# Performance work log

Measured on AMD Instinct MI355X. Metric: run time of the kernel, lower is better.

Reference implementation:

```python
import jax, jax.numpy as jnp
import numpy as np

ALPHA = 0.2  # tf.nn.leaky_relu default alpha
B, LATENT, T, N = 8, 256, 128, 768
F, L, E = 4, 3, 12288


def _causal_conv1d(x, w, b):
    # x: [B,T,Cin], w: [K,Cin,Cout] -> causal pad left by K-1
    k = w.shape[0]
    y = jax.lax.conv_general_dilated(x, w, (1,), ((k - 1, 0),),
                                     dimension_numbers=('NWC', 'WIO', 'NWC'))
    return y + b


def _same_conv1d(x, w, b):
    y = jax.lax.conv_general_dilated(x, w, (1,), 'SAME',
                                     dimension_numbers=('NWC', 'WIO', 'NWC'))
    return y + b


def _same_conv2d(x, w, b):
    y = jax.lax.conv_general_dilated(x, w, (1, 1), 'SAME',
                                     dimension_numbers=('NHWC', 'HWIO', 'NHWC'))
    return y + b


def _gat(nodes, row, col, qw, qb, kw, kb, vw, vb):
    # tf_geometric-style single-head GAT; row/col already contain self-loops.
    M = nodes.shape[0]
    Q = jax.nn.leaky_relu(nodes @ qw + qb, ALPHA)
    K = jax.nn.leaky_relu(nodes @ kw + kb, ALPHA)
    V = nodes @ vw
    scale = jnp.sqrt(jnp.asarray(Q.shape[-1], nodes.dtype))
    score = jnp.sum(Q[row] * K[col], axis=-1) / scale  # [E']
    smax = jax.ops.segment_max(score, row, num_segments=M)
    ex = jnp.exp(score - smax[row])
    den = jax.ops.segment_sum(ex, row, num_segments=M)
    att = ex / den[row]
    out = jax.ops.segment_sum(V[col] * att[:, None], row, num_segments=M)
    return out + vb


def _gw_layer(y, row, col, wa, ba, wb, bb, qw, qb, kw, kb, vw, vb, rw, rb):
    b_, t_, n_, f_ = y.shape
    x = jnp.moveaxis(y, -1, 0)  # [F,B,T,N]

    def branch(xf, wa_, ba_, wb_, bb_, qw_, qb_, kw_, kb_, vw_, vb_):
        a = jax.nn.sigmoid(_causal_conv1d(xf, wa_, ba_))
        g = a * jnp.tanh(_causal_conv1d(xf, wb_, bb_))   # gated TCN [B,T,N]
        nodes = g.transpose(0, 2, 1).reshape(b_ * n_, t_)  # node id = b*N + n
        h = _gat(nodes, row, col, qw_, qb_, kw_, kb_, vw_, vb_)
        return h.reshape(b_, n_, t_).transpose(0, 2, 1)  # [B,T,N]

    outs = jax.vmap(branch)(x, wa, ba, wb, bb, qw, qb, kw, kb, vw, vb)
    outs = jnp.moveaxis(outs, 0, -1)                      # [B,T,N,F]
    res = jnp.einsum('btnf,fg->btng', y, rw) + rb         # 1x1 res conv
    return outs + res


def _decoder(x, edges, shunt_dense_w, shunt_dense_b, shunt_c1_w, shunt_c1_b,
             shunt_c2_w, shunt_c2_b, tcn_a_w, tcn_a_b, tcn_b_w, tcn_b_b,
             gat_q_w, gat_q_b, gat_k_w, gat_k_b, gat_v_w, gat_v_b,
             res_w, res_b, skip_w, skip_b, out1_w, out1_b, out2_w, out2_b):
    # ConvShunt: [B,latent] -> [B,T] -> [B,T,N] -> [B,T,N,F]
    y = x @ shunt_dense_w + shunt_dense_b
    y = _same_conv1d(y[..., None], shunt_c1_w, shunt_c1_b)
    y = _same_conv2d(y[..., None], shunt_c2_w, shunt_c2_b)
    M = B * N
    self_idx = jnp.arange(M, dtype=edges.dtype)
    row = jnp.concatenate([edges[0], self_idx])
    col = jnp.concatenate([edges[1], self_idx])
    skips = []
    for i in range(L):
        y = _gw_layer(y, row, col, tcn_a_w[i], tcn_a_b[i], tcn_b_w[i], tcn_b_b[i],
                      gat_q_w[i], gat_q_b[i], gat_k_w[i], gat_k_b[i],
                      gat_v_w[i], gat_v_b[i], res_w[i], res_b[i])
        skips.append(jax.nn.leaky_relu(
            jnp.einsum('btnf,f->btn', y, skip_w[i]) + skip_b[i], ALPHA))
    s = jnp.stack(skips, axis=-1)                         # [B,T,N,L]
    g = jax.nn.leaky_relu(_same_conv2d(s, out1_w, out1_b), ALPHA)
    return _same_conv2d(g, out2_w, out2_b)                # [B,T,N,1]


def setup_inputs() -> dict:
    ks = iter(jax.random.split(jax.random.key(0), 32))

    def w(shape, fan_in):
        return jax.random.normal(next(ks), shape, jnp.float32) / np.sqrt(fan_in).astype(np.float32)

    return {
        'x': jax.random.normal(next(ks), (B, LATENT), jnp.float32),
        'edges': jax.random.randint(next(ks), (2, E), 0, N, jnp.int32),
        'shunt_dense_w': w((LATENT, T), LATENT),
        'shunt_dense_b': jnp.zeros((T,), jnp.float32),
        'shunt_c1_w': w((3, 1, N), 3),
        'shunt_c1_b': jnp.zeros((N,), jnp.float32),
        'shunt_c2_w': w((3, 3, 1, F), 9),
        'shunt_c2_b': jnp.zeros((F,), jnp.float32),
        'tcn_a_w': w((L, F, 5, N, N), 5 * N),
        'tcn_a_b': jnp.zeros((L, F, N), jnp.float32),
        'tcn_b_w': w((L, F, 5, N, N), 5 * N),
        'tcn_b_b': jnp.zeros((L, F, N), jnp.float32),
        'gat_q_w': w((L, F, T, T), T),
        'gat_q_b': jnp.zeros((L, F, T), jnp.float32),
        'gat_k_w': w((L, F, T, T), T),
        'gat_k_b': jnp.zeros((L, F, T), jnp.float32),
        'gat_v_w': w((L, F, T, T), T),
        'gat_v_b': jnp.zeros((L, F, T), jnp.float32),
        'res_w': w((L, F, F), F),
        'res_b': jnp.zeros((L, F), jnp.float32),
        'skip_w': w((L, F), F),
        'skip_b': jnp.zeros((L,), jnp.float32),
        'out1_w': w((3, 3, L, 1), 9 * L),
        'out1_b': jnp.zeros((1,), jnp.float32),
        'out2_w': w((1, 1, 1, 1), 1),
        'out2_b': jnp.zeros((1,), jnp.float32),
    }


def reference(x, edges, shunt_dense_w, shunt_dense_b, shunt_c1_w, shunt_c1_b,
              shunt_c2_w, shunt_c2_b, tcn_a_w, tcn_a_b, tcn_b_w, tcn_b_b,
              gat_q_w, gat_q_b, gat_k_w, gat_k_b, gat_v_w, gat_v_b,
              res_w, res_b, skip_w, skip_b, out1_w, out1_b, out2_w, out2_b):
    return _decoder(x, edges, shunt_dense_w, shunt_dense_b, shunt_c1_w, shunt_c1_b,
                    shunt_c2_w, shunt_c2_b, tcn_a_w, tcn_a_b, tcn_b_w, tcn_b_b,
                    gat_q_w, gat_q_b, gat_k_w, gat_k_b, gat_v_w, gat_v_b,
                    res_w, res_b, skip_w, skip_b, out1_w, out1_b, out2_w, out2_b)
```

## Files before the change

### kernel.cpp

```cpp
#include <hip/hip_runtime.h>
#include <math.h>

#define ALPHA_ 0.2f
#define AS1 __attribute__((address_space(1)))
#define AS3 __attribute__((address_space(3)))

constexpr int B_ = 8, LATENT_ = 256, T_ = 128, N_ = 768, F_ = 4, L_ = 3, E_ = 12288;
constexpr int M_ = B_ * N_;
constexpr int MT_ = B_ * T_;
constexpr int EP_ = E_ + M_;
constexpr int BTN_ = B_ * T_ * N_;
constexpr size_t SZ_ = (size_t)BTN_ * F_;
constexpr int KTCN_ = 5 * N_;
constexpr int KSPLIT_ = KTCN_ / 2;
constexpr int TP_ = T_ + 4;

typedef __bf16 bf16x8 __attribute__((ext_vector_type(8)));
typedef float f32x4 __attribute__((ext_vector_type(4)));

__device__ __forceinline__ float lrelu(float x) { return x > 0.0f ? x : ALPHA_ * x; }
__device__ __forceinline__ unsigned short f2bf(float x) {
    union { __bf16 h; unsigned short u; } c; c.h = (__bf16)x; return c.u;
}
__device__ __forceinline__ float bf2f(unsigned short u) {
    return __uint_as_float(((unsigned)u) << 16);
}

__global__ void k_dense(const float* __restrict__ x, const float* __restrict__ w,
                        const float* __restrict__ b, float* __restrict__ y0) {
    int i = blockIdx.x * blockDim.x + threadIdx.x;
    if (i >= B_ * T_) return;
    int bb = i / T_, t = i % T_;
    float acc = b[t];
    for (int l = 0; l < LATENT_; ++l) acc += x[bb * LATENT_ + l] * w[l * T_ + t];
    y0[i] = acc;
}

__global__ void k_conv1(const float* __restrict__ y0, const float* __restrict__ w,
                        const float* __restrict__ b, float* __restrict__ y1) {
    int i = blockIdx.x * blockDim.x + threadIdx.x;
    if (i >= BTN_) return;
    int n = i % N_, t = (i / N_) % T_, bb = i / (N_ * T_);
    float acc = b[n];
    #pragma unroll
    for (int k = 0; k < 3; ++k) {
        int tt = t - 1 + k;
        if (tt >= 0 && tt < T_) acc += y0[bb * T_ + tt] * w[k * N_ + n];
    }
    y1[i] = acc;
}

__global__ void k_conv2w(const float* __restrict__ y1, const float* __restrict__ w,
                         const float* __restrict__ b, float* __restrict__ y,
                         unsigned short* __restrict__ xTpad) {
    int i = blockIdx.x * blockDim.x + threadIdx.x;
    if (i >= BTN_) return;
    int n = i % N_, t = (i / N_) % T_, bb = i / (N_ * T_);
    float acc[F_];
    #pragma unroll
    for (int f = 0; f < F_; ++f) acc[f] = b[f];
    #pragma unroll
    for (int dt = 0; dt < 3; ++dt) {
        int tt = t - 1 + dt;
        if (tt < 0 || tt >= T_) continue;
        #pragma unroll
        for (int dn = 0; dn < 3; ++dn) {
            int nn = n - 1 + dn;
            if (nn < 0 || nn >= N_) continue;
            float v = y1[(bb * T_ + tt) * N_ + nn];
            #pragma unroll
            for (int f = 0; f < F_; ++f) acc[f] += v * w[(dt * 3 + dn) * F_ + f];
        }
    }
    #pragma unroll
    for (int f = 0; f < F_; ++f) {
        y[(size_t)i * F_ + f] = acc[f];
        xTpad[((size_t)(f * B_ + bb) * TP_ + 4 + t) * N_ + n] = f2bf(acc[f]);
    }
}

__global__ __launch_bounds__(256) void k_convT2(const float* __restrict__ aw,
        const float* __restrict__ bw, unsigned short* __restrict__ wat3,
        unsigned short* __restrict__ wbt3) {
    __shared__ float tl[64][33];
    const int z = blockIdx.z;
    const int f = z & 3, wsel = (z >> 2) & 1, layer = z >> 3;
    const size_t toff = ((size_t)layer * F_ + f) * KTCN_ * N_;
    const float* in = (wsel ? bw : aw) + toff;
    unsigned short* outT = (wsel ? wbt3 : wat3) + toff;
    const int n0 = blockIdx.x * 32, k0 = blockIdx.y * 64;
    const int tx = threadIdx.x & 31, ty = threadIdx.x >> 5;
    #pragma unroll
    for (int r = 0; r < 8; ++r)
        tl[ty + r * 8][tx] = in[(size_t)(k0 + ty + r * 8) * N_ + n0 + tx];
    __syncthreads();
    const int kx2 = threadIdx.x & 63, ny = threadIdx.x >> 6;
    #pragma unroll
    for (int r = 0; r < 8; ++r)
        outT[(size_t)(n0 + ny + r * 4) * KTCN_ + k0 + kx2] = f2bf(tl[kx2][ny + r * 4]);
}

__global__ __launch_bounds__(256) void k_convTproj(const float* __restrict__ qw,
        const float* __restrict__ kw, const float* __restrict__ vw,
        unsigned short* __restrict__ pwt3) {
    __shared__ float tl[32][33];
    const int z = blockIdx.z;
    const int f = z & 3;
    const int sel = (z >> 2) % 3;
    const int layer = z / 12;
    const float* in = (sel == 0 ? qw : (sel == 1 ? kw : vw))
                      + ((size_t)layer * F_ + f) * T_ * T_;
    unsigned short* outT = pwt3 + (((size_t)layer * 3 + sel) * F_ + f) * T_ * T_;
    const int x0 = blockIdx.x * 32;
    const int y0 = blockIdx.y * 32;
    const int tx = threadIdx.x & 31, ty = threadIdx.x >> 5;
    #pragma unroll
    for (int r = 0; r < 4; ++r)
        tl[ty + r * 8][tx] = in[(size_t)(y0 + ty + r * 8) * T_ + x0 + tx];
    __syncthreads();
    #pragma unroll
    for (int r = 0; r < 4; ++r)
        outT[(size_t)(x0 + ty + r * 8) * T_ + y0 + tx] = f2bf(tl[tx][ty + r * 8]);
}

__global__ __launch_bounds__(256) void k_tcn_mfma(
        const unsigned short* __restrict__ xTpad,
        const unsigned short* __restrict__ wat, const unsigned short* __restrict__ wbt,
        const float* __restrict__ ba, const float* __restrict__ bbias,
        unsigned short* __restrict__ oa0, unsigned short* __restrict__ oa1,
        unsigned short* __restrict__ ob0, unsigned short* __restrict__ ob1) {
    __shared__ unsigned short As[128 * 32];
    __shared__ unsigned short Bs[128 * 32];
    const int bid = blockIdx.x;
    const int bt = bid / 96;
    const int c = bid - bt * 96;
    const int xb = c % 6;
    const int zz = c / 6;
    const int f = zz & 3;
    const int wsel = (zz >> 2) & 1;
    const int s = zz >> 3;
    const int n0 = xb * 128;
    const unsigned short* xf = xTpad + (size_t)(f * B_ + bt) * TP_ * N_;
    const unsigned short* wf = (wsel ? wbt : wat) + (size_t)f * N_ * KTCN_ + (size_t)n0 * KTCN_;
    const float* bias = (wsel ? bbias : ba) + f * N_;
    unsigned short* out = (wsel ? (s ? ob1 : ob0) : (s ? oa1 : oa0));
    const int tid = threadIdx.x;
    const int lane = tid & 63;
    const int w = tid >> 6;
    const int wm = (w >> 1) * 64, wn = (w & 1) * 64;
    const int r16 = lane & 15, kb = lane >> 4;
    const int srow = lane >> 2;
    const int scol = (((lane & 3) ^ ((lane >> 3) & 3)) * 8);
    const int kx = (kb ^ ((r16 >> 1) & 3)) * 8;
    f32x4 acc[4][4] = {};
    const int k_lo = s * KSPLIT_, k_hi = k_lo + KSPLIT_;
    for (int kk0 = k_lo; kk0 < k_hi; kk0 += 32) {
        const int ks = kk0 / N_;
        const int nin0 = kk0 - ks * N_;
        #pragma unroll
        for (int h = 0; h < 2; ++h) {
            const int seg = w + 4 * h;
            const int row = seg * 16 + srow;
            const unsigned short* gA = xf + (size_t)(row + ks) * N_ + nin0 + scol;
            const unsigned short* gB = wf + (size_t)row * KTCN_ + kk0 + scol;
            __builtin_amdgcn_global_load_lds((const AS1 unsigned int*)(const void*)gA,
                    (AS3 unsigned int*)(void*)(As + seg * 512), 16, 0, 0);
            __builtin_amdgcn_global_load_lds((const AS1 unsigned int*)(const void*)gB,
                    (AS3 unsigned int*)(void*)(Bs + seg * 512), 16, 0, 0);
        }
        __syncthreads();
        bf16x8 av[4], bv[4];
        #pragma unroll
        for (int i = 0; i < 4; ++i) av[i] = *(const bf16x8*)(As + (wm + i * 16 + r16) * 32 + kx);
        #pragma unroll
        for (int j = 0; j < 4; ++j) bv[j] = *(const bf16x8*)(Bs + (wn + j * 16 + r16) * 32 + kx);
        #pragma unroll
        for (int i = 0; i < 4; ++i)
            #pragma unroll
            for (int j = 0; j < 4; ++j)
                acc[i][j] = __builtin_amdgcn_mfma_f32_16x16x32_bf16(av[i], bv[j], acc[i][j], 0, 0, 0);
        __syncthreads();
    }
    unsigned short* of = out + (size_t)(f * B_ + bt) * T_ * N_;
    #pragma unroll
    for (int i = 0; i < 4; ++i) {
        #pragma unroll
        for (int j = 0; j < 4; ++j) {
            const int n = n0 + wn + j * 16 + r16;
            const float bv2 = (s == 0) ? bias[n] : 0.0f;
            #pragma unroll
            for (int r = 0; r < 4; ++r) {
                const int m = wm + i * 16 + kb * 4 + r;
                of[(size_t)m * N_ + n] = f2bf(acc[i][j][r] + bv2);
            }
        }
    }
}

__global__ __launch_bounds__(256) void k_gate_nodes(const unsigned short* __restrict__ a0,
        const unsigned short* __restrict__ a1, const unsigned short* __restrict__ b0,
        const unsigned short* __restrict__ b1, unsigned short* __restrict__ nodes) {
    __shared__ float tl[32][33];
    const int bz = blockIdx.z;
    const int t0 = blockIdx.x * 32, n0 = blockIdx.y * 32;
    const int tx = threadIdx.x & 31, ty = threadIdx.x >> 5;
    const size_t base = (size_t)bz * T_ * N_;
    #pragma unroll
    for (int r = 0; r < 4; ++r) {
        const size_t idx = base + (size_t)(t0 + ty + r * 8) * N_ + n0 + tx;
        const float av = bf2f(a0[idx]) + bf2f(a1[idx]);
        const float bvv = bf2f(b0[idx]) + bf2f(b1[idx]);
        tl[ty + r * 8][tx] = (1.0f / (1.0f + __expf(-av))) * tanhf(bvv);
    }
    __syncthreads();
    #pragma unroll
    for (int r = 0; r < 4; ++r)
        nodes[base + (size_t)(n0 + ty + r * 8) * T_ + t0 + tx] = f2bf(tl[tx][ty + r * 8]);
}

__global__ __launch_bounds__(256) void k_proj_mfma(
        const unsigned short* __restrict__ nodes, const unsigned short* __restrict__ pwt,
        const float* __restrict__ qb, const float* __restrict__ kbias,
        unsigned short* __restrict__ Q, unsigned short* __restrict__ K,
        unsigned short* __restrict__ V) {
    __shared__ unsigned short As[128 * 32];
    __shared__ unsigned short Bs[128 * 32];
    const int zz = blockIdx.z;
    const int f = zz & 3;
    const int sel = zz >> 2;
    const int m0 = blockIdx.y * 128;
    const unsigned short* af = nodes + (size_t)f * M_ * T_;
    const unsigned short* wfp = pwt + (size_t)sel * F_ * T_ * T_ + (size_t)f * T_ * T_;
    const float* bias = (sel == 0) ? qb : (sel == 1 ? kbias : nullptr);
    unsigned short* out = (sel == 0) ? Q : (sel == 1 ? K : V);
    const int tid = threadIdx.x;
    const int lane = tid & 63;
    const int w = tid >> 6;
    const int wm = (w >> 1) * 64, wn = (w & 1) * 64;
    const int r16 = lane & 15, kb = lane >> 4;
    const int srow = lane >> 2;
    const int scol = (((lane & 3) ^ ((lane >> 3) & 3)) * 8);
    const int kx = (kb ^ ((r16 >> 1) & 3)) * 8;
    f32x4 acc[4][4] = {};
    for (int kk0 = 0; kk0 < T_; kk0 += 32) {
        #pragma unroll
        for (int h = 0; h < 2; ++h) {
            const int seg = w + 4 * h;
            const int row = seg * 16 + srow;
            const unsigned short* gA = af + (size_t)(m0 + row) * T_ + kk0 + scol;
            const unsigned short* gB = wfp + (size_t)row * T_ + kk0 + scol;
            __builtin_amdgcn_global_load_lds((const AS1 unsigned int*)(const void*)gA,
                    (AS3 unsigned int*)(void*)(As + seg * 512), 16, 0, 0);
            __builtin_amdgcn_global_load_lds((const AS1 unsigned int*)(const void*)gB,
                    (AS3 unsigned int*)(void*)(Bs + seg * 512), 16, 0, 0);
        }
        __syncthreads();
        bf16x8 av[4], bv[4];
        #pragma unroll
        for (int i = 0; i < 4; ++i) av[i] = *(const bf16x8*)(As + (wm + i * 16 + r16) * 32 + kx);
        #pragma unroll
        for (int j = 0; j < 4; ++j) bv[j] = *(const bf16x8*)(Bs + (wn + j * 16 + r16) * 32 + kx);
        #pragma unroll
        for (int i = 0; i < 4; ++i)
            #pragma unroll
            for (int j = 0; j < 4; ++j)
                acc[i][j] = __builtin_amdgcn_mfma_f32_16x16x32_bf16(av[i], bv[j], acc[i][j], 0, 0, 0);
        __syncthreads();
    }
    const int do_l = (sel < 2);
    unsigned short* of = out + (size_t)f * M_ * T_;
    #pragma unroll
    for (int i = 0; i < 4; ++i) {
        #pragma unroll
        for (int j = 0; j < 4; ++j) {
            const int n = wn + j * 16 + r16;
            #pragma unroll
            for (int r = 0; r < 4; ++r) {
                const int m = m0 + wm + i * 16 + kb * 4 + r;
                float v = acc[i][j][r];
                if (bias) v += bias[f * T_ + n];
                if (do_l) v = lrelu(v);
                of[(size_t)m * T_ + n] = f2bf(v);
            }
        }
    }
}

__device__ __forceinline__ int edge_row(const int* e, int i) { return i < E_ ? e[i] : i - E_; }
__device__ __forceinline__ int edge_col(const int* e, int i) { return i < E_ ? e[E_ + i] : i - E_; }

__global__ void k_hist(const int* __restrict__ edges, int* __restrict__ deg) {
    int i = blockIdx.x * blockDim.x + threadIdx.x;
    if (i >= EP_) return;
    atomicAdd(&deg[edge_row(edges, i)], 1);
}

__global__ __launch_bounds__(256) void k_scan(const int* __restrict__ deg,
        int* __restrict__ rowptr, int* __restrict__ cursor) {
    __shared__ int part[256];
    const int tid = threadIdx.x;
    constexpr int PER = M_ / 256;
    int loc[PER];
    int s = 0;
    #pragma unroll
    for (int j = 0; j < PER; ++j) { loc[j] = s; s += deg[tid * PER + j]; }
    part[tid] = s;
    __syncthreads();
    if (tid == 0) {
        int run = 0;
        for (int i2 = 0; i2 < 256; ++i2) { int v = part[i2]; part[i2] = run; run += v; }
        rowptr[M_] = run;
    }
    __syncthreads();
    const int off = part[tid];
    #pragma unroll
    for (int j = 0; j < PER; ++j) {
        rowptr[tid * PER + j] = off + loc[j];
        cursor[tid * PER + j] = off + loc[j];
    }
}

__global__ void k_scatter(const int* __restrict__ edges, int* __restrict__ cursor,
                          int* __restrict__ csr_col) {
    int i = blockIdx.x * blockDim.x + threadIdx.x;
    if (i >= EP_) return;
    int r = edge_row(edges, i), c = edge_col(edges, i);
    int pos = atomicAdd(&cursor[r], 1);
    csr_col[pos] = c;
}

__global__ __launch_bounds__(256) void k_gat(const unsigned short* __restrict__ Q,
        const unsigned short* __restrict__ Kb, const unsigned short* __restrict__ V,
        const int* __restrict__ rowptr, const int* __restrict__ csr_col,
        unsigned short* __restrict__ H) {
    constexpr int CAP = 128;
    __shared__ float sc[4][CAP];
    const int w = threadIdx.x >> 6, lane = threadIdx.x & 63;
    const int wv = blockIdx.x * 4 + w;
    const int f = wv / M_, r = wv - f * M_;
    const int p0 = rowptr[r], p1 = rowptr[r + 1];
    const unsigned short* Qr = Q + ((size_t)f * M_ + r) * T_;
    const float q0 = bf2f(Qr[lane]), q1 = bf2f(Qr[lane + 64]);
    float mx = -3.4e38f;
    for (int j = p0; j < p1; ++j) {
        const unsigned short* Kc = Kb + ((size_t)f * M_ + csr_col[j]) * T_;
        float s = q0 * bf2f(Kc[lane]) + q1 * bf2f(Kc[lane + 64]);
        #pragma unroll
        for (int mk = 32; mk >= 1; mk >>= 1) s += __shfl_xor(s, mk);
        s *= 0.0883883476483184f;
        if (lane == 0 && j - p0 < CAP) sc[w][j - p0] = s;
        mx = fmaxf(mx, s);
    }
    float den = 0.0f;
    for (int j = p0; j < p1; ++j) {
        float s;
        if (j - p0 < CAP) s = sc[w][j - p0];
        else {
            const unsigned short* Kc = Kb + ((size_t)f * M_ + csr_col[j]) * T_;
            s = q0 * bf2f(Kc[lane]) + q1 * bf2f(Kc[lane + 64]);
            #pragma unroll
            for (int mk = 32; mk >= 1; mk >>= 1) s += __shfl_xor(s, mk);
            s *= 0.0883883476483184f;
        }
        den += __expf(s - mx);
    }
    const float rden = 1.0f / den;
    float a0 = 0.0f, a1 = 0.0f;
    for (int j = p0; j < p1; ++j) {
        const int c = csr_col[j];
        float s;
        if (j - p0 < CAP) s = sc[w][j - p0];
        else {
            const unsigned short* Kc = Kb + ((size_t)f * M_ + c) * T_;
            s = q0 * bf2f(Kc[lane]) + q1 * bf2f(Kc[lane + 64]);
            #pragma unroll
            for (int mk = 32; mk >= 1; mk >>= 1) s += __shfl_xor(s, mk);
            s *= 0.0883883476483184f;
        }
        const float att = __expf(s - mx) * rden;
        const unsigned short* Vc = V + ((size_t)f * M_ + c) * T_;
        a0 += att * bf2f(Vc[lane]);
        a1 += att * bf2f(Vc[lane + 64]);
    }
    unsigned short* Hr = H + ((size_t)f * M_ + r) * T_;
    Hr[lane] = f2bf(a0);
    Hr[lane + 64] = f2bf(a1);
}

__global__ __launch_bounds__(256) void k_combine_t(const float* __restrict__ y,
        const unsigned short* __restrict__ H, const float* __restrict__ vb,
        const float* __restrict__ rw, const float* __restrict__ rb,
        const float* __restrict__ skw, const float* __restrict__ skb, int layer,
        float* __restrict__ ynext, unsigned short* __restrict__ xTpad,
        float* __restrict__ sbufp) {
    __shared__ float hl[F_][32][33];
    const int b = blockIdx.z;
    const int t0 = blockIdx.x * 32, n0 = blockIdx.y * 32;
    const int tx = threadIdx.x & 31, ty = threadIdx.x >> 5;
    #pragma unroll
    for (int g = 0; g < F_; ++g)
        #pragma unroll
        for (int r = 0; r < 4; ++r) {
            const int nn = ty + r * 8;
            hl[g][nn][tx] = bf2f(H[((size_t)g * M_ + b * N_ + n0 + nn) * T_ + t0 + tx]);
        }
    __syncthreads();
    #pragma unroll
    for (int r = 0; r < 4; ++r) {
        const int tt = ty + r * 8;
        const int t = t0 + tt;
        const size_t i = ((size_t)b * T_ + t) * N_ + n0 + tx;
        const float4 y4 = *(const float4*)(y + i * 4);
        float o[F_];
        #pragma unroll
        for (int g = 0; g < F_; ++g) {
            float acc = hl[g][tx][tt] + vb[g * T_ + t] + rb[g];
            acc += y4.x * rw[0 * F_ + g] + y4.y * rw[1 * F_ + g]
                 + y4.z * rw[2 * F_ + g] + y4.w * rw[3 * F_ + g];
            o[g] = acc;
        }
        float4 o4 = {o[0], o[1], o[2], o[3]};
        *(float4*)(ynext + i * 4) = o4;
        #pragma unroll
        for (int g = 0; g < F_; ++g)
            xTpad[((size_t)(g * B_ + b) * TP_ + 4 + t) * N_ + n0 + tx] = f2bf(o[g]);
        float sk = skb[layer];
        #pragma unroll
        for (int g = 0; g < F_; ++g) sk += o[g] * skw[layer * F_ + g];
        sbufp[(size_t)layer * BTN_ + i] = lrelu(sk);
    }
}

__global__ void k_final(const float* __restrict__ sbufp, const float* __restrict__ o1w,
        const float* __restrict__ o1b, const float* __restrict__ o2w,
        const float* __restrict__ o2b, float* __restrict__ out) {
    int i = blockIdx.x * blockDim.x + threadIdx.x;
    if (i >= BTN_) return;
    int n = i % N_, t = (i / N_) % T_, bb = i / (N_ * T_);
    float acc = o1b[0];
    #pragma unroll
    for (int dt = 0; dt < 3; ++dt) {
        int tt = t - 1 + dt;
        if (tt < 0 || tt >= T_) continue;
        #pragma unroll
        for (int dn = 0; dn < 3; ++dn) {
            int nn = n - 1 + dn;
            if (nn < 0 || nn >= N_) continue;
            const size_t base = (size_t)(bb * T_ + tt) * N_ + nn;
            #pragma unroll
            for (int l = 0; l < L_; ++l)
                acc += sbufp[(size_t)l * BTN_ + base] * o1w[(dt * 3 + dn) * L_ + l];
        }
    }
    float g = lrelu(acc);
    out[i] = g * o2w[0] + o2b[0];
}

extern "C" void kernel_launch(void* const* d_in, const int* in_sizes, int n_in,
                              void* d_out, int out_size, void* d_ws, size_t ws_size,
                              hipStream_t stream) {
    const float* x       = (const float*)d_in[0];
    const int*   edges   = (const int*)d_in[1];
    const float* sd_w    = (const float*)d_in[2];
    const float* sd_b    = (const float*)d_in[3];
    const float* c1w     = (const float*)d_in[4];
    const float* c1b     = (const float*)d_in[5];
    const float* c2w     = (const float*)d_in[6];
    const float* c2b     = (const float*)d_in[7];
    const float* tcn_a_w = (const float*)d_in[8];
    const float* tcn_a_b = (const float*)d_in[9];
    const float* tcn_b_w = (const float*)d_in[10];
    const float* tcn_b_b = (const float*)d_in[11];
    const float* gat_q_w = (const float*)d_in[12];
    const float* gat_q_b = (const float*)d_in[13];
    const float* gat_k_w = (const float*)d_in[14];
    const float* gat_k_b = (const float*)d_in[15];
    const float* gat_v_w = (const float*)d_in[16];
    const float* gat_v_b = (const float*)d_in[17];
    const float* res_w   = (const float*)d_in[18];
    const float* res_b   = (const float*)d_in[19];
    const float* skip_w  = (const float*)d_in[20];
    const float* skip_b  = (const float*)d_in[21];
    const float* out1_w  = (const float*)d_in[22];
    const float* out1_b  = (const float*)d_in[23];
    const float* out2_w  = (const float*)d_in[24];
    const float* out2_b  = (const float*)d_in[25];
    float* out = (float*)d_out;

    float* ws = (float*)d_ws;
    size_t off = 0;
    auto alloc = [&](size_t nf) { float* p = ws + off; off += nf; return p; };
    float* ybuf  = alloc(SZ_);
    float* y2buf = alloc(SZ_);
    float* sbufp = alloc((size_t)BTN_ * L_);
    float* y0    = alloc(MT_);
    float* y1    = alloc(BTN_);
    unsigned short* xTpad  = (unsigned short*)alloc((size_t)F_ * B_ * TP_ * N_ / 2 + 16);
    unsigned short* nodesb = (unsigned short*)alloc(SZ_ / 2);
    unsigned short* qb16   = (unsigned short*)alloc(SZ_ / 2);
    unsigned short* kb16   = (unsigned short*)alloc(SZ_ / 2);
    unsigned short* vb16   = (unsigned short*)alloc(SZ_ / 2);
    unsigned short* Hb     = (unsigned short*)alloc(SZ_ / 2);
    unsigned short* pa0    = (unsigned short*)alloc(SZ_ / 2);
    unsigned short* pa1    = (unsigned short*)alloc(SZ_ / 2);
    unsigned short* pb0    = (unsigned short*)alloc(SZ_ / 2);
    unsigned short* pb1    = (unsigned short*)alloc(SZ_ / 2);
    unsigned short* wat3 = (unsigned short*)alloc((size_t)L_ * F_ * KTCN_ * N_ / 2);
    unsigned short* wbt3 = (unsigned short*)alloc((size_t)L_ * F_ * KTCN_ * N_ / 2);
    unsigned short* pwt3 = (unsigned short*)alloc((size_t)L_ * 3 * F_ * T_ * T_ / 2);
    int* rowptr  = (int*)alloc(M_ + 1);
    int* cursor  = (int*)alloc(M_);
    int* deg     = (int*)alloc(M_);
    int* csr_col = (int*)alloc(EP_);
    (void)ws_size; (void)in_sizes; (void)n_in; (void)out_size;

    hipMemsetAsync(xTpad, 0, (size_t)F_ * B_ * TP_ * N_ * 2, stream);
    hipMemsetAsync(deg, 0, M_ * 4, stream);
    k_hist<<<(EP_ + 255) / 256, 256, 0, stream>>>(edges, deg);
    k_scan<<<1, 256, 0, stream>>>(deg, rowptr, cursor);
    k_scatter<<<(EP_ + 255) / 256, 256, 0, stream>>>(edges, cursor, csr_col);

    dim3 gw2(N_ / 32, KTCN_ / 64, 8 * L_);
    k_convT2<<<gw2, 256, 0, stream>>>(tcn_a_w, tcn_b_w, wat3, wbt3);
    dim3 gpw(T_ / 32, T_ / 32, 12 * L_);
    k_convTproj<<<gpw, 256, 0, stream>>>(gat_q_w, gat_k_w, gat_v_w, pwt3);

    k_dense<<<(B_ * T_ + 255) / 256, 256, 0, stream>>>(x, sd_w, sd_b, y0);
    k_conv1<<<(BTN_ + 255) / 256, 256, 0, stream>>>(y0, c1w, c1b, y1);
    k_conv2w<<<(BTN_ + 255) / 256, 256, 0, stream>>>(y1, c2w, c2b, ybuf, xTpad);

    float* cur = ybuf;
    float* nxt = y2buf;
    for (int layer = 0; layer < L_; ++layer) {
        const float* ba = tcn_a_b + (size_t)layer * F_ * N_;
        const float* bb = tcn_b_b + (size_t)layer * F_ * N_;
        const float* qb = gat_q_b + (size_t)layer * F_ * T_;
        const float* kbias = gat_k_b + (size_t)layer * F_ * T_;
        const float* vb = gat_v_b + (size_t)layer * F_ * T_;
        const float* rw = res_w + (size_t)layer * F_ * F_;
        const float* rb = res_b + (size_t)layer * F_;
        const unsigned short* wat = wat3 + (size_t)layer * F_ * KTCN_ * N_;
        const unsigned short* wbt = wbt3 + (size_t)layer * F_ * KTCN_ * N_;
        const unsigned short* pwt = pwt3 + (size_t)layer * 3 * F_ * T_ * T_;

        k_tcn_mfma<<<768, 256, 0, stream>>>(xTpad, wat, wbt, ba, bb, pa0, pa1, pb0, pb1);
        dim3 gg(T_ / 32, N_ / 32, F_ * B_);
        k_gate_nodes<<<gg, 256, 0, stream>>>(pa0, pa1, pb0, pb1, nodesb);
        dim3 gp(1, M_ / 128, 12);
        k_proj_mfma<<<gp, 256, 0, stream>>>(nodesb, pwt, qb, kbias, qb16, kb16, vb16);
        k_gat<<<(F_ * M_) / 4, 256, 0, stream>>>(qb16, kb16, vb16, rowptr, csr_col, Hb);
        dim3 gc(T_ / 32, N_ / 32, B_);
        k_combine_t<<<gc, 256, 0, stream>>>(cur, Hb, vb, rw, rb, skip_w, skip_b,
                layer, nxt, xTpad, sbufp);
        float* tmp = cur; cur = nxt; nxt = tmp;
    }
    k_final<<<(BTN_ + 255) / 256, 256, 0, stream>>>(sbufp, out1_w, out1_b, out2_w, out2_b, out);
}
```

Baseline: 577.5 us.

## Split TCN GEMM K dimension four ways and vectorize weight transpose

The TCN MFMA kernel now splits its K reduction into four parts instead of two, doubling the grid to 1536 blocks so more CUs have work. The gate kernel sums four bf16 partials per element, which adds partial-buffer write and read traffic. The weight transpose kernel is also reworked to use 64x64 tiles with float4 loads and 16-byte packed bf16 stores, cutting the number of memory transactions in that one-time conversion.

Result: slower. 610.6 us (+5.7%).

```diff
diff --git a/kernel.cpp b/kernel.cpp
--- a/kernel.cpp
+++ b/kernel.cpp
@@ -12,7 +12,7 @@
 constexpr int BTN_ = B_ * T_ * N_;
 constexpr size_t SZ_ = (size_t)BTN_ * F_;
 constexpr int KTCN_ = 5 * N_;
-constexpr int KSPLIT_ = KTCN_ / 2;
+constexpr int KS4_ = KTCN_ / 4;
 constexpr int TP_ = T_ + 4;
 
 typedef __bf16 bf16x8 __attribute__((ext_vector_type(8)));
@@ -82,22 +82,36 @@
 __global__ __launch_bounds__(256) void k_convT2(const float* __restrict__ aw,
         const float* __restrict__ bw, unsigned short* __restrict__ wat3,
         unsigned short* __restrict__ wbt3) {
-    __shared__ float tl[64][33];
+    __shared__ float tl[64 * 65];
     const int z = blockIdx.z;
     const int f = z & 3, wsel = (z >> 2) & 1, layer = z >> 3;
-    const size_t toff = ((size_t)layer * F_ + f) * KTCN_ * N_;
+    const size_t toff = ((size_t)layer * F_ + f) * (size_t)KTCN_ * N_;
     const float* in = (wsel ? bw : aw) + toff;
     unsigned short* outT = (wsel ? wbt3 : wat3) + toff;
-    const int n0 = blockIdx.x * 32, k0 = blockIdx.y * 64;
-    const int tx = threadIdx.x & 31, ty = threadIdx.x >> 5;
-    #pragma unroll
-    for (int r = 0; r < 8; ++r)
-        tl[ty + r * 8][tx] = in[(size_t)(k0 + ty + r * 8) * N_ + n0 + tx];
+    const int n0 = blockIdx.x * 64, k0 = blockIdx.y * 64;
+    const int tid = threadIdx.x;
+    const int lr = tid >> 4;
+    const int lc4 = (tid & 15) * 4;
+    #pragma unroll
+    for (int r = 0; r < 4; ++r) {
+        const int k = lr + r * 16;
+        const float4 v = *(const float4*)(in + (size_t)(k0 + k) * N_ + n0 + lc4);
+        tl[k * 65 + lc4 + 0] = v.x;
+        tl[k * 65 + lc4 + 1] = v.y;
+        tl[k * 65 + lc4 + 2] = v.z;
+        tl[k * 65 + lc4 + 3] = v.w;
+    }
     __syncthreads();
-    const int kx2 = threadIdx.x & 63, ny = threadIdx.x >> 6;
-    #pragma unroll
-    for (int r = 0; r < 8; ++r)
-        outT[(size_t)(n0 + ny + r * 4) * KTCN_ + k0 + kx2] = f2bf(tl[kx2][ny + r * 4]);
+    const int sr = tid >> 3;
+    const int sc8 = (tid & 7) * 8;
+    #pragma unroll
+    for (int r = 0; r < 2; ++r) {
+        const int n = sr + r * 32;
+        unsigned short pk[8];
+        #pragma unroll
+        for (int i = 0; i < 8; ++i) pk[i] = f2bf(tl[(sc8 + i) * 65 + n]);
+        *(uint4*)(outT + (size_t)(n0 + n) * KTCN_ + k0 + sc8) = *(uint4*)pk;
+    }
 }
 
 __global__ __launch_bounds__(256) void k_convTproj(const float* __restrict__ qw,
@@ -127,13 +141,12 @@
         const unsigned short* __restrict__ xTpad,
         const unsigned short* __restrict__ wat, const unsigned short* __restrict__ wbt,
         const float* __restrict__ ba, const float* __restrict__ bbias,
-        unsigned short* __restrict__ oa0, unsigned short* __restrict__ oa1,
-        unsigned short* __restrict__ ob0, unsigned short* __restrict__ ob1) {
+        unsigned short* __restrict__ pa, unsigned short* __restrict__ pb) {
     __shared__ unsigned short As[128 * 32];
     __shared__ unsigned short Bs[128 * 32];
     const int bid = blockIdx.x;
-    const int bt = bid / 96;
-    const int c = bid - bt * 96;
+    const int bt = bid / 192;
+    const int c = bid - bt * 192;
     const int xb = c % 6;
     const int zz = c / 6;
     const int f = zz & 3;
@@ -143,7 +156,7 @@
     const unsigned short* xf = xTpad + (size_t)(f * B_ + bt) * TP_ * N_;
     const unsigned short* wf = (wsel ? wbt : wat) + (size_t)f * N_ * KTCN_ + (size_t)n0 * KTCN_;
     const float* bias = (wsel ? bbias : ba) + f * N_;
-    unsigned short* out = (wsel ? (s ? ob1 : ob0) : (s ? oa1 : oa0));
+    unsigned short* out = (wsel ? pb : pa) + (size_t)s * SZ_;
     const int tid = threadIdx.x;
     const int lane = tid & 63;
     const int w = tid >> 6;
@@ -153,7 +166,7 @@
     const int scol = (((lane & 3) ^ ((lane >> 3) & 3)) * 8);
     const int kx = (kb ^ ((r16 >> 1) & 3)) * 8;
     f32x4 acc[4][4] = {};
-    const int k_lo = s * KSPLIT_, k_hi = k_lo + KSPLIT_;
+    const int k_lo = s * KS4_, k_hi = k_lo + KS4_;
     for (int kk0 = k_lo; kk0 < k_hi; kk0 += 32) {
         const int ks = kk0 / N_;
         const int nin0 = kk0 - ks * N_;
@@ -197,9 +210,8 @@
     }
 }
 
-__global__ __launch_bounds__(256) void k_gate_nodes(const unsigned short* __restrict__ a0,
-        const unsigned short* __restrict__ a1, const unsigned short* __restrict__ b0,
-        const unsigned short* __restrict__ b1, unsigned short* __restrict__ nodes) {
+__global__ __launch_bounds__(256) void k_gate_nodes(const unsigned short* __restrict__ pa,
+        const unsigned short* __restrict__ pb, unsigned short* __restrict__ nodes) {
     __shared__ float tl[32][33];
     const int bz = blockIdx.z;
     const int t0 = blockIdx.x * 32, n0 = blockIdx.y * 32;
@@ -208,8 +220,12 @@
     #pragma unroll
     for (int r = 0; r < 4; ++r) {
         const size_t idx = base + (size_t)(t0 + ty + r * 8) * N_ + n0 + tx;
-        const float av = bf2f(a0[idx]) + bf2f(a1[idx]);
-        const float bvv = bf2f(b0[idx]) + bf2f(b1[idx]);
+        float av = 0.0f, bvv = 0.0f;
+        #pragma unroll
+        for (int s = 0; s < 4; ++s) {
+            av += bf2f(pa[(size_t)s * SZ_ + idx]);
+            bvv += bf2f(pb[(size_t)s * SZ_ + idx]);
+        }
         tl[ty + r * 8][tx] = (1.0f / (1.0f + __expf(-av))) * tanhf(bvv);
     }
     __syncthreads();
@@ -501,10 +517,8 @@
     unsigned short* kb16   = (unsigned short*)alloc(SZ_ / 2);
     unsigned short* vb16   = (unsigned short*)alloc(SZ_ / 2);
     unsigned short* Hb     = (unsigned short*)alloc(SZ_ / 2);
-    unsigned short* pa0    = (unsigned short*)alloc(SZ_ / 2);
-    unsigned short* pa1    = (unsigned short*)alloc(SZ_ / 2);
-    unsigned short* pb0    = (unsigned short*)alloc(SZ_ / 2);
-    unsigned short* pb1    = (unsigned short*)alloc(SZ_ / 2);
+    unsigned short* pa     = (unsigned short*)alloc(SZ_ * 2);
+    unsigned short* pb     = (unsigned short*)alloc(SZ_ * 2);
     unsigned short* wat3 = (unsigned short*)alloc((size_t)L_ * F_ * KTCN_ * N_ / 2);
     unsigned short* wbt3 = (unsigned short*)alloc((size_t)L_ * F_ * KTCN_ * N_ / 2);
     unsigned short* pwt3 = (unsigned short*)alloc((size_t)L_ * 3 * F_ * T_ * T_ / 2);
@@ -520,7 +534,7 @@
     k_scan<<<1, 256, 0, stream>>>(deg, rowptr, cursor);
     k_scatter<<<(EP_ + 255) / 256, 256, 0, stream>>>(edges, cursor, csr_col);
 
-    dim3 gw2(N_ / 32, KTCN_ / 64, 8 * L_);
+    dim3 gw2(N_ / 64, KTCN_ / 64, 8 * L_);
     k_convT2<<<gw2, 256, 0, stream>>>(tcn_a_w, tcn_b_w, wat3, wbt3);
     dim3 gpw(T_ / 32, T_ / 32, 12 * L_);
     k_convTproj<<<gpw, 256, 0, stream>>>(gat_q_w, gat_k_w, gat_v_w, pwt3);
@@ -543,9 +557,9 @@
         const unsigned short* wbt = wbt3 + (size_t)layer * F_ * KTCN_ * N_;
         const unsigned short* pwt = pwt3 + (size_t)layer * 3 * F_ * T_ * T_;
 
-        k_tcn_mfma<<<768, 256, 0, stream>>>(xTpad, wat, wbt, ba, bb, pa0, pa1, pb0, pb1);
+        k_tcn_mfma<<<1536, 256, 0, stream>>>(xTpad, wat, wbt, ba, bb, pa, pb);
         dim3 gg(T_ / 32, N_ / 32, F_ * B_);
-        k_gate_nodes<<<gg, 256, 0, stream>>>(pa0, pa1, pb0, pb1, nodesb);
+        k_gate_nodes<<<gg, 256, 0, stream>>>(pa, pb, nodesb);
         dim3 gp(1, M_ / 128, 12);
         k_proj_mfma<<<gp, 256, 0, stream>>>(nodesb, pwt, qb, kbias, qb16, kb16, vb16);
         k_gat<<<(F_ * M_) / 4, 256, 0, stream>>>(qb16, kb16, vb16, rowptr, csr_col, Hb);
```
